# Kernel optimization log

Measured on AMD Instinct MI355X. Metric: run time of the kernel, lower is better.

The kernel has to match this reference:

```python
import jax, jax.numpy as jnp
import numpy as np

D_MODEL = 1024
N_HEADS = 16
D_K = D_MODEL // N_HEADS
FF_DIM = 4096
EPS = 1e-6
NEG = -1.0e9


def _layernorm(x, g, b):
    # torch: a_2 * (x - mean) / (std + eps) + b_2, std is unbiased (ddof=1)
    mean = jnp.mean(x, axis=-1, keepdims=True)
    std = jnp.std(x, axis=-1, keepdims=True, ddof=1)
    return g * (x - mean) / (std + EPS) + b


def setup_inputs() -> dict:
    key = jax.random.key(0)
    ks = jax.random.split(key, 8)
    s = 0.02
    x = jax.random.normal(ks[0], (2, 2048, D_MODEL), dtype=jnp.float32)
    mask = jnp.ones((2, 1, 1, 2048), dtype=jnp.int32)
    return {
        "x": x,
        "mask": mask,
        "wq": jax.random.normal(ks[1], (D_MODEL, D_MODEL), jnp.float32) * s,
        "wk": jax.random.normal(ks[2], (D_MODEL, D_MODEL), jnp.float32) * s,
        "wv": jax.random.normal(ks[3], (D_MODEL, D_MODEL), jnp.float32) * s,
        "wo": jax.random.normal(ks[4], (D_MODEL, D_MODEL), jnp.float32) * s,
        "bq": jnp.zeros((D_MODEL,), jnp.float32),
        "bk": jnp.zeros((D_MODEL,), jnp.float32),
        "bv": jnp.zeros((D_MODEL,), jnp.float32),
        "bo": jnp.zeros((D_MODEL,), jnp.float32),
        "w1": jax.random.normal(ks[5], (D_MODEL, FF_DIM), jnp.float32) * s,
        "b1": jnp.zeros((FF_DIM,), jnp.float32),
        "w2": jax.random.normal(ks[6], (FF_DIM, D_MODEL), jnp.float32) * s,
        "b2": jnp.zeros((D_MODEL,), jnp.float32),
        "ln1_g": jnp.ones((D_MODEL,), jnp.float32),
        "ln1_b": jnp.zeros((D_MODEL,), jnp.float32),
        "ln2_g": jnp.ones((D_MODEL,), jnp.float32),
        "ln2_b": jnp.zeros((D_MODEL,), jnp.float32),
    }


def reference(x, mask, wq, wk, wv, wo, bq, bk, bv, bo, w1, b1, w2, b2,
              ln1_g, ln1_b, ln2_g, ln2_b):
    B, S, _ = x.shape
    # --- sublayer 1: pre-norm self-attention with residual ---
    h = _layernorm(x, ln1_g, ln1_b)
    q = (h @ wq + bq).reshape(B, S, N_HEADS, D_K).transpose(0, 2, 1, 3)
    k = (h @ wk + bk).reshape(B, S, N_HEADS, D_K).transpose(0, 2, 1, 3)
    v = (h @ wv + bv).reshape(B, S, N_HEADS, D_K).transpose(0, 2, 1, 3)
    scores = jnp.einsum('bhqd,bhkd->bhqk', q, k) / np.sqrt(D_K).astype(np.float32)
    scores = jnp.where(mask == 0, NEG, scores)
    attn = jax.nn.softmax(scores, axis=-1)
    ctx = jnp.einsum('bhqk,bhkd->bhqd', attn, v)
    ctx = ctx.transpose(0, 2, 1, 3).reshape(B, S, D_MODEL)
    x = x + (ctx @ wo + bo)
    # --- sublayer 2: pre-norm FFN with residual ---
    h2 = _layernorm(x, ln2_g, ln2_b)
    ff = jax.nn.relu(h2 @ w1 + b1) @ w2 + b2
    return x + ff
```

## Files before the change

### kernel.cpp

```cpp
#include <hip/hip_runtime.h>

typedef unsigned short u16;
typedef unsigned int u32;
typedef __attribute__((ext_vector_type(8))) short bf16x8;
typedef __attribute__((ext_vector_type(4))) float f32x4;

__device__ __forceinline__ u16 f2bf(float f) {
  union { float f; unsigned int u; } x;
  x.f = f;
  unsigned int r = x.u + 0x7fffu + ((x.u >> 16) & 1u);
  return (u16)(r >> 16);
}

__device__ __forceinline__ float bf2f(u16 v) {
  union { unsigned int u; float f; } x;
  x.u = ((unsigned int)v) << 16;
  return x.f;
}

__device__ __forceinline__ u32 fbits(float f) {
  union { float f; u32 u; } x; x.f = f; return x.u;
}

__device__ __forceinline__ void async16(const u16* g, u16* l) {
  __builtin_amdgcn_global_load_lds((const __attribute__((address_space(1))) void*)g,
                                   (__attribute__((address_space(3))) void*)l, 16, 0, 0);
}

__device__ __forceinline__ void stage128x64(const u16* __restrict__ src, long row0, int k0,
                                            int ld, u16* lds, int wave, int lane) {
#pragma unroll
  for (int r = 0; r < 4; ++r) {
    int s = r * 256 + wave * 64 + lane;
    int row = s >> 3;
    int c = (s & 7) ^ (row & 7);
    async16(src + (row0 + row) * (long)ld + k0 + c * 8, lds + (r * 256 + wave * 64) * 8);
  }
}

__device__ __forceinline__ void stage_half512(const u16* __restrict__ src, long row0, int k0,
                                              int ld, u16* lbase, int wave, int lane) {
#pragma unroll
  for (int r = 0; r < 2; ++r) {
    int s = r * 512 + wave * 64 + lane;
    int row = s >> 3;
    int c = (s & 7) ^ (row & 7);
    async16(src + (row0 + row) * (long)ld + k0 + c * 8, lbase + (r * 512 + wave * 64) * 8);
  }
}

__device__ __forceinline__ void stage64x128(const u16* __restrict__ src, int col0, int ld,
                                            u16* lds, int wave, int lane) {
#pragma unroll
  for (int r = 0; r < 4; ++r) {
    int s = r * 256 + wave * 64 + lane;
    int row = s >> 4;
    int c = (s & 15) ^ (row & 15);
    async16(src + (long)row * ld + col0 + c * 8, lds + (r * 256 + wave * 64) * 8);
  }
}

__device__ __forceinline__ void ln_core(float4 v, const float* g, const float* b, int t,
                                        u16* outrow) {
  float s = v.x + v.y + v.z + v.w;
  float ss = v.x * v.x + v.y * v.y + v.z * v.z + v.w * v.w;
#pragma unroll
  for (int off = 32; off; off >>= 1) {
    s += __shfl_xor(s, off);
    ss += __shfl_xor(ss, off);
  }
  __shared__ float red[8];
  int wave = t >> 6, lane = t & 63;
  if (lane == 0) { red[wave] = s; red[wave + 4] = ss; }
  __syncthreads();
  float tot = red[0] + red[1] + red[2] + red[3];
  float tots = red[4] + red[5] + red[6] + red[7];
  float mean = tot * (1.0f / 1024.0f);
  float var = (tots - 1024.0f * mean * mean) * (1.0f / 1023.0f);
  var = fmaxf(var, 0.0f);
  float inv = 1.0f / (sqrtf(var) + 1e-6f);
  float4 gv = ((const float4*)g)[t];
  float4 bv = ((const float4*)b)[t];
  union { unsigned long long u64; u16 h[4]; } o;
  o.h[0] = f2bf(gv.x * (v.x - mean) * inv + bv.x);
  o.h[1] = f2bf(gv.y * (v.y - mean) * inv + bv.y);
  o.h[2] = f2bf(gv.z * (v.z - mean) * inv + bv.z);
  o.h[3] = f2bf(gv.w * (v.w - mean) * inv + bv.w);
  *(unsigned long long*)(outrow + t * 4) = o.u64;
}

__global__ __launch_bounds__(256) void prep(const float* __restrict__ wq,
                                            const float* __restrict__ wk,
                                            const float* __restrict__ wv,
                                            const float* __restrict__ wo,
                                            const float* __restrict__ w1,
                                            const float* __restrict__ w2,
                                            const float* __restrict__ x,
                                            const float* __restrict__ ln1_g,
                                            const float* __restrict__ ln1_b,
                                            u16* __restrict__ wqkvT,
                                            u16* __restrict__ w1T,
                                            u16* __restrict__ w2T,
                                            u16* __restrict__ hout) {
  const int bid = blockIdx.x;
  const int part = bid >> 12;
  const int local = bid & 4095;
  const int t = threadIdx.x;
  if (part == 1) {
    float4 v = ((const float4*)(x + (long)local * 1024))[t];
    ln_core(v, ln1_g, ln1_b, t, hout + (long)local * 1024);
    return;
  }
  __shared__ float tile[32][33];
  const float* src; u16* dst; int C, R, bx, by;
  if (part == 0) {
    int sub = local >> 10;
    src = sub == 0 ? wq : (sub == 1 ? wk : (sub == 2 ? wv : wo));
    dst = wqkvT + (long)sub * 1024 * 1024;
    C = 1024; R = 1024; bx = local & 31; by = (local >> 5) & 31;
  } else if (part == 2) {
    src = w1; dst = w1T; C = 4096; R = 1024; bx = local & 127; by = local >> 7;
  } else {
    src = w2; dst = w2T; C = 1024; R = 4096; bx = local & 31; by = local >> 5;
  }
  int c0 = bx * 32, r0 = by * 32;
  int tx = t & 31, ty = t >> 5;
#pragma unroll
  for (int i = 0; i < 32; i += 8)
    tile[ty + i][tx] = src[(long)(r0 + ty + i) * C + c0 + tx];
  __syncthreads();
#pragma unroll
  for (int i = 0; i < 32; i += 8)
    dst[(long)(c0 + ty + i) * R + r0 + tx] = f2bf(tile[tx][ty + i]);
}

__global__ __launch_bounds__(256) void ln_fuse(const float* x, const float* bres,
                                               const u16* p0, const u16* p1,
                                               const u16* p2, const u16* p3,
                                               const float* g, const float* b,
                                               float* yout, u16* hout) {
  int row = blockIdx.x, t = threadIdx.x;
  long base = (long)row * 1024;
  float4 xv = ((const float4*)(x + base))[t];
  float4 bo = ((const float4*)bres)[t];
  ushort4 a = ((const ushort4*)(p0 + base))[t];
  ushort4 c = ((const ushort4*)(p1 + base))[t];
  ushort4 d = ((const ushort4*)(p2 + base))[t];
  ushort4 e = ((const ushort4*)(p3 + base))[t];
  float4 y;
  y.x = xv.x + bo.x + (bf2f(a.x) + bf2f(c.x)) + (bf2f(d.x) + bf2f(e.x));
  y.y = xv.y + bo.y + (bf2f(a.y) + bf2f(c.y)) + (bf2f(d.y) + bf2f(e.y));
  y.z = xv.z + bo.z + (bf2f(a.z) + bf2f(c.z)) + (bf2f(d.z) + bf2f(e.z));
  y.w = xv.w + bo.w + (bf2f(a.w) + bf2f(c.w)) + (bf2f(d.w) + bf2f(e.w));
  ((float4*)(yout + base))[t] = y;
  ln_core(y, g, b, t, hout + base);
}

__global__ __launch_bounds__(256) void final_add(float* __restrict__ out,
                                                 const float* __restrict__ b2,
                                                 const u16* __restrict__ p0,
                                                 const u16* __restrict__ p1,
                                                 const u16* __restrict__ p2) {
  int row = blockIdx.x, t = threadIdx.x;
  long base = (long)row * 1024;
  float4 o = ((float4*)(out + base))[t];
  float4 bb = ((const float4*)b2)[t];
  ushort4 a = ((const ushort4*)(p0 + base))[t];
  ushort4 c = ((const ushort4*)(p1 + base))[t];
  ushort4 d = ((const ushort4*)(p2 + base))[t];
  o.x += bb.x + (bf2f(a.x) + bf2f(c.x)) + bf2f(d.x);
  o.y += bb.y + (bf2f(a.y) + bf2f(c.y)) + bf2f(d.y);
  o.z += bb.z + (bf2f(a.z) + bf2f(c.z)) + bf2f(d.z);
  o.w += bb.w + (bf2f(a.w) + bf2f(c.w)) + bf2f(d.w);
  ((float4*)(out + base))[t] = o;
}

template <int MODE, int SWZ>
__global__ __launch_bounds__(512, 1) void gemm8(const u16* __restrict__ A,
                                                const u16* __restrict__ Bt, int M, int N, int K,
                                                void* __restrict__ outp,
                                                const float* __restrict__ bias,
                                                const float* __restrict__ bias1,
                                                const float* __restrict__ bias2,
                                                u16* __restrict__ q_out, u16* __restrict__ k_out,
                                                u16* __restrict__ v_out) {
  __shared__ __align__(16) u16 lds[65536];
  (void)M;
  const int tid = threadIdx.x;
  const int wave = tid >> 6, lane = tid & 63;
  const int lane16 = lane & 15, quad = lane >> 4;
  const int wr2 = wave >> 2, wc2 = wave & 3;
  int bx = blockIdx.x, by = blockIdx.y;
  if (SWZ) {
    const int fid = by * gridDim.x + bx;
    const int xcd = fid & 7, slot = fid >> 3;
    const int nxh = gridDim.x >> 1;
    bx = (xcd & 1) * nxh + slot % nxh;
    by = (xcd >> 1) * 4 + slot / nxh;
  }
  const long m0 = (long)by * 256;
  const long n0 = (long)bx * 256;
  const int kLen = K / gridDim.z;
  const int kBeg = blockIdx.z * kLen;
  const int nT = kLen >> 6;

  u16* const ldsA = lds;
  u16* const ldsB = lds + 32768;

  const f32x4 fzero = {0.f, 0.f, 0.f, 0.f};
  f32x4 acc[2][2][4][2];
#pragma unroll
  for (int qa = 0; qa < 2; ++qa)
#pragma unroll
    for (int qb = 0; qb < 2; ++qb)
#pragma unroll
      for (int m = 0; m < 4; ++m)
#pragma unroll
        for (int n = 0; n < 2; ++n) acc[qa][qb][m][n] = fzero;

  stage_half512(A,  m0,       kBeg,      K, ldsA,                 wave, lane);
  stage_half512(Bt, n0,       kBeg,      K, ldsB,                 wave, lane);
  stage_half512(Bt, n0 + 128, kBeg,      K, ldsB + 8192,          wave, lane);
  stage_half512(A,  m0 + 128, kBeg,      K, ldsA + 8192,          wave, lane);
  stage_half512(A,  m0,       kBeg + 64, K, ldsA + 16384,         wave, lane);
  stage_half512(Bt, n0,       kBeg + 64, K, ldsB + 16384,         wave, lane);
  stage_half512(Bt, n0 + 128, kBeg + 64, K, ldsB + 16384 + 8192,  wave, lane);
  asm volatile("s_waitcnt vmcnt(10)" ::: "memory");
  asm volatile("s_barrier" ::: "memory");

  for (int t = 0; t < nT; ++t) {
    u16* const aB = ldsA + (t & 1) * 16384;
    u16* const bB = ldsB + (t & 1) * 16384;
    u16* const aN1 = ldsA + ((t + 1) & 1) * 16384;
    const int k1 = kBeg + (t + 1 < nT ? t + 1 : nT - 1) * 64;
    const int k2 = kBeg + (t + 2 < nT ? t + 2 : nT - 1) * 64;

    bf16x8 af[4][2], b0f[2][2], b1f[2][2];

#pragma unroll
    for (int m = 0; m < 4; ++m) {
      const int row = wr2 * 64 + m * 16 + lane16;
#pragma unroll
      for (int kk = 0; kk < 2; ++kk)
        af[m][kk] = *(const bf16x8*)(aB + row * 64 + (((kk * 4 + quad) ^ (row & 7)) << 3));
    }
#pragma unroll
    for (int n = 0; n < 2; ++n) {
      const int row = wc2 * 32 + n * 16 + lane16;
#pragma unroll
      for (int kk = 0; kk < 2; ++kk)
        b0f[n][kk] = *(const bf16x8*)(bB + row * 64 + (((kk * 4 + quad) ^ (row & 7)) << 3));
    }
    stage_half512(A, m0 + 128, k1, K, aN1 + 8192, wave, lane);
    asm volatile("s_barrier" ::: "memory");
    asm volatile("s_waitcnt lgkmcnt(0)" ::: "memory");
    __builtin_amdgcn_sched_barrier(0);
    __builtin_amdgcn_s_setprio(1);
#pragma unroll
    for (int m = 0; m < 4; ++m)
#pragma unroll
      for (int n = 0; n < 2; ++n) {
        acc[0][0][m][n] = __builtin_amdgcn_mfma_f32_16x16x32_bf16(af[m][0], b0f[n][0], acc[0][0][m][n], 0, 0, 0);
        acc[0][0][m][n] = __builtin_amdgcn_mfma_f32_16x16x32_bf16(af[m][1], b0f[n][1], acc[0][0][m][n], 0, 0, 0);
      }
    __builtin_amdgcn_s_setprio(0);
    asm volatile("s_waitcnt vmcnt(10)" ::: "memory");
    asm volatile("s_barrier" ::: "memory");

#pragma unroll
    for (int n = 0; n < 2; ++n) {
      const int row = 128 + wc2 * 32 + n * 16 + lane16;
#pragma unroll
      for (int kk = 0; kk < 2; ++kk)
        b1f[n][kk] = *(const bf16x8*)(bB + row * 64 + (((kk * 4 + quad) ^ (row & 7)) << 3));
    }
    stage_half512(A, m0, k2, K, aB, wave, lane);
    asm volatile("s_barrier" ::: "memory");
    asm volatile("s_waitcnt lgkmcnt(0)" ::: "memory");
    __builtin_amdgcn_sched_barrier(0);
    __builtin_amdgcn_s_setprio(1);
#pragma unroll
    for (int m = 0; m < 4; ++m)
#pragma unroll
      for (int n = 0; n < 2; ++n) {
        acc[0][1][m][n] = __builtin_amdgcn_mfma_f32_16x16x32_bf16(af[m][0], b1f[n][0], acc[0][1][m][n], 0, 0, 0);
        acc[0][1][m][n] = __builtin_amdgcn_mfma_f32_16x16x32_bf16(af[m][1], b1f[n][1], acc[0][1][m][n], 0, 0, 0);
      }
    __builtin_amdgcn_s_setprio(0);
    asm volatile("s_waitcnt vmcnt(10)" ::: "memory");
    asm volatile("s_barrier" ::: "memory");

#pragma unroll
    for (int m = 0; m < 4; ++m) {
      const int row = 128 + wr2 * 64 + m * 16 + lane16;
#pragma unroll
      for (int kk = 0; kk < 2; ++kk)
        af[m][kk] = *(const bf16x8*)(aB + row * 64 + (((kk * 4 + quad) ^ (row & 7)) << 3));
    }
    stage_half512(Bt, n0, k2, K, bB, wave, lane);
    asm volatile("s_barrier" ::: "memory");
    asm volatile("s_waitcnt lgkmcnt(0)" ::: "memory");
    __builtin_amdgcn_sched_barrier(0);
    __builtin_amdgcn_s_setprio(1);
#pragma unroll
    for (int m = 0; m < 4; ++m)
#pragma unroll
      for (int n = 0; n < 2; ++n) {
        acc[1][1][m][n] = __builtin_amdgcn_mfma_f32_16x16x32_bf16(af[m][0], b1f[n][0], acc[1][1][m][n], 0, 0, 0);
        acc[1][1][m][n] = __builtin_amdgcn_mfma_f32_16x16x32_bf16(af[m][1], b1f[n][1], acc[1][1][m][n], 0, 0, 0);
      }
    __builtin_amdgcn_s_setprio(0);
    asm volatile("s_waitcnt vmcnt(10)" ::: "memory");
    asm volatile("s_barrier" ::: "memory");

    stage_half512(Bt, n0 + 128, k2, K, bB + 8192, wave, lane);
    asm volatile("s_barrier" ::: "memory");
    __builtin_amdgcn_s_setprio(1);
#pragma unroll
    for (int m = 0; m < 4; ++m)
#pragma unroll
      for (int n = 0; n < 2; ++n) {
        acc[1][0][m][n] = __builtin_amdgcn_mfma_f32_16x16x32_bf16(af[m][0], b0f[n][0], acc[1][0][m][n], 0, 0, 0);
        acc[1][0][m][n] = __builtin_amdgcn_mfma_f32_16x16x32_bf16(af[m][1], b0f[n][1], acc[1][0][m][n], 0, 0, 0);
      }
    __builtin_amdgcn_s_setprio(0);
    asm volatile("s_waitcnt vmcnt(10)" ::: "memory");
    asm volatile("s_barrier" ::: "memory");
  }

  asm volatile("s_waitcnt vmcnt(0)" ::: "memory");

  if (MODE == 0) {
    const int sel = (int)(n0 >> 10);
    if (sel == 2) {
#pragma unroll
      for (int qa = 0; qa < 2; ++qa)
#pragma unroll
        for (int qb = 0; qb < 2; ++qb) {
          __syncthreads();
#pragma unroll
          for (int n = 0; n < 2; ++n) {
            const int lcol = wc2 * 32 + n * 16 + lane16;
            const float bvj = bias2[(int)(n0 - 2048) + qb * 128 + lcol];
#pragma unroll
            for (int m = 0; m < 4; ++m)
#pragma unroll
              for (int r = 0; r < 4; ++r) {
                const int lrow = wr2 * 64 + m * 16 + quad * 4 + r;
                lds[lcol * 136 + lrow] = f2bf(acc[qa][qb][m][n][r] + bvj);
              }
          }
          __syncthreads();
          const int lcol = tid >> 2, seg = tid & 3;
          const int cc = (int)(n0 - 2048) + qb * 128 + lcol;
          const int head = cc >> 6, d = cc & 63;
          const int bI = (int)((m0 + qa * 128) >> 11);
          const int s0 = (int)((m0 + qa * 128) & 2047);
          u16* dst = v_out + ((long)(bI * 16 + head) * 64 + d) * 2048 + s0 + seg * 32;
          const u16* s = lds + lcol * 136 + seg * 32;
#pragma unroll
          for (int c2 = 0; c2 < 4; ++c2) ((uint4*)dst)[c2] = ((const uint4*)s)[c2];
        }
      return;
    }
    u16* qk = sel == 0 ? q_out : k_out;
    const float* bb = sel == 0 ? bias : bias1;
#pragma unroll
    for (int qa = 0; qa < 2; ++qa)
#pragma unroll
      for (int qb = 0; qb < 2; ++qb)
#pragma unroll
        for (int n = 0; n < 2; ++n) {
          const int col = (int)n0 + qb * 128 + wc2 * 32 + n * 16 + lane16;
          const int cc = col & 1023;
          const float bv = bb[cc];
          const int head = cc >> 6, d = cc & 63;
#pragma unroll
          for (int m = 0; m < 4; ++m) {
            const int rw = (int)m0 + qa * 128 + wr2 * 64 + m * 16 + quad * 4;
#pragma unroll
            for (int r = 0; r < 4; ++r) {
              const int row = rw + r;
              const int bI = row >> 11, sS = row & 2047;
              const long bh = (long)bI * 16 + head;
              float vv = acc[qa][qb][m][n][r] + bv;
              if (sel == 0) vv *= 0.18033688f;
              qk[(bh * 2048 + sS) * 64 + d] = f2bf(vv);
            }
          }
        }
  } else if (MODE == 2) {
    u16* op = (u16*)outp;
#pragma unroll
    for (int qa = 0; qa < 2; ++qa)
#pragma unroll
      for (int qb = 0; qb < 2; ++qb)
#pragma unroll
        for (int n = 0; n < 2; ++n) {
          const int col = (int)n0 + qb * 128 + wc2 * 32 + n * 16 + lane16;
          const float bv = bias[col];
#pragma unroll
          for (int m = 0; m < 4; ++m) {
            const long rbase = ((long)m0 + qa * 128 + wr2 * 64 + m * 16 + quad * 4) * N + col;
#pragma unroll
            for (int r = 0; r < 4; ++r)
              op[rbase + (long)r * N] = f2bf(fmaxf(acc[qa][qb][m][n][r] + bv, 0.0f));
          }
        }
  } else {
    const int z = blockIdx.z;
    if (MODE == 3 && z == 3) {
      float* op = (float*)v_out;
#pragma unroll
      for (int qa = 0; qa < 2; ++qa)
#pragma unroll
        for (int qb = 0; qb < 2; ++qb)
#pragma unroll
          for (int n = 0; n < 2; ++n) {
            const int col = (int)n0 + qb * 128 + wc2 * 32 + n * 16 + lane16;
#pragma unroll
            for (int m = 0; m < 4; ++m) {
              const long rbase = ((long)m0 + qa * 128 + wr2 * 64 + m * 16 + quad * 4) * N + col;
#pragma unroll
              for (int r = 0; r < 4; ++r)
                unsafeAtomicAdd(op + rbase + (long)r * N, acc[qa][qb][m][n][r]);
            }
          }
    } else {
      u16* pp = z == 0 ? (u16*)outp : (z == 1 ? q_out : (z == 2 ? k_out : v_out));
#pragma unroll
      for (int qa = 0; qa < 2; ++qa)
#pragma unroll
        for (int qb = 0; qb < 2; ++qb)
#pragma unroll
          for (int n = 0; n < 2; ++n) {
            const int col = (int)n0 + qb * 128 + wc2 * 32 + n * 16 + lane16;
#pragma unroll
            for (int m = 0; m < 4; ++m) {
              const long rbase = ((long)m0 + qa * 128 + wr2 * 64 + m * 16 + quad * 4) * N + col;
#pragma unroll
              for (int r = 0; r < 4; ++r)
                pp[rbase + (long)r * N] = f2bf(acc[qa][qb][m][n][r]);
            }
          }
    }
  }
}

#define FA_C0 28.854239f
__global__ __launch_bounds__(256) void flash_attn(const u16* __restrict__ q,
                                                  const u16* __restrict__ k,
                                                  const u16* __restrict__ v,
                                                  const int* __restrict__ mask,
                                                  u16* __restrict__ ctx) {
  const int fid = blockIdx.y * 16 + blockIdx.x;
  const int xcd = fid & 7, slot = fid >> 3;
  const int bh = xcd * 4 + (slot >> 4);
  const int q0 = (slot & 15) * 128;
  const int b = bh >> 4, h = bh & 15;
  const int tid = threadIdx.x;
  const int wave = tid >> 6, lane = tid & 63;
  const int lane16 = lane & 15, quad = lane >> 4;

  const u16* qp = q + (long)bh * 2048 * 64;
  const u16* kp = k + (long)bh * 2048 * 64;
  const u16* vp = v + (long)bh * 64 * 2048;
  const int* mp = mask + b * 2048;

  __shared__ __align__(16) u16 ldsK[128 * 64];
  __shared__ __align__(16) u16 ldsVT[64 * 128];
  __shared__ __align__(16) u16 ldsP23[2 * 4096];
  __shared__ __align__(16) float ldsMask[128];
  __shared__ int ldsFlag[2];
  u16* myP = (wave < 2) ? (ldsK + wave * 4096) : (ldsP23 + (wave - 2) * 4096);

  bf16x8 qf[2][2];
#pragma unroll
  for (int g = 0; g < 2; ++g) {
    const long qrow = q0 + wave * 32 + g * 16 + lane16;
    qf[g][0] = *(const bf16x8*)(qp + qrow * 64 + quad * 8);
    qf[g][1] = *(const bf16x8*)(qp + qrow * 64 + 32 + quad * 8);
  }

  const f32x4 fzero = {0.f, 0.f, 0.f, 0.f};
  const f32x4 cC0 = {-FA_C0, -FA_C0, -FA_C0, -FA_C0};
  float l_loc[2] = {0.f, 0.f};
  f32x4 o_acc[2][4];
#pragma unroll
  for (int g = 0; g < 2; ++g)
#pragma unroll
    for (int j = 0; j < 4; ++j) o_acc[g][j] = fzero;

  const int xorm = (lane16 & 7) << 2;
  u16* const pw0 = myP + lane16 * 128;
  u16* const pw1 = myP + (16 + lane16) * 128;

  for (int kt = 0; kt < 2048; kt += 128) {
    stage128x64(kp, kt, 0, 64, ldsK, wave, lane);
    stage64x128(vp, kt, 2048, ldsVT, wave, lane);
    if (tid < 128) {
      int mv = mp[kt + tid];
      ldsMask[tid] = (mv == 0) ? -1.0e9f : 0.0f;
      unsigned long long bal = __ballot(mv != 0);
      if ((tid & 63) == 0) ldsFlag[tid >> 6] = (bal == ~0ull) ? 1 : 0;
    }
    __syncthreads();
    const bool allv = (ldsFlag[0] & ldsFlag[1]) != 0;

    f32x4 s_acc[8][2];
    __builtin_amdgcn_s_setprio(1);
#pragma unroll
    for (int j = 0; j < 8; ++j) {
      int row = j * 16 + lane16;
      int c0i = quad ^ (row & 7);
      int c1i = (4 + quad) ^ (row & 7);
      bf16x8 kf0 = *(const bf16x8*)(ldsK + row * 64 + c0i * 8);
      bf16x8 kf1 = *(const bf16x8*)(ldsK + row * 64 + c1i * 8);
#pragma unroll
      for (int g = 0; g < 2; ++g) {
        f32x4 sa = __builtin_amdgcn_mfma_f32_16x16x32_bf16(kf0, qf[g][0], cC0, 0, 0, 0);
        sa = __builtin_amdgcn_mfma_f32_16x16x32_bf16(kf1, qf[g][1], sa, 0, 0, 0);
        s_acc[j][g] = sa;
      }
    }
    __builtin_amdgcn_s_setprio(0);
    __syncthreads();

#pragma unroll
    for (int j = 0; j < 8; ++j) {
      int cw = ((4 * j + quad) ^ xorm) * 4;
#pragma unroll
      for (int g = 0; g < 2; ++g) {
        f32x4 sa = s_acc[j][g];
        if (!allv) {
          f32x4 mk = *(const f32x4*)(ldsMask + j * 16 + quad * 4);
          sa = sa + mk;
        }
        float p0 = __builtin_exp2f(sa[0]);
        float p1 = __builtin_exp2f(sa[1]);
        float p2 = __builtin_exp2f(sa[2]);
        float p3 = __builtin_exp2f(sa[3]);
        l_loc[g] += (p0 + p1) + (p2 + p3);
        uint2 pk;
        pk.x = __builtin_amdgcn_perm(fbits(p1), fbits(p0), 0x07060302u);
        pk.y = __builtin_amdgcn_perm(fbits(p3), fbits(p2), 0x07060302u);
        *(uint2*)((g ? pw1 : pw0) + cw) = pk;
      }
    }
    __builtin_amdgcn_s_setprio(1);
#pragma unroll
    for (int kk = 0; kk < 4; ++kk) {
      int cr = ((8 * kk + 2 * quad) ^ xorm) * 4;
      bf16x8 pf0 = *(const bf16x8*)(pw0 + cr);
      bf16x8 pf1 = *(const bf16x8*)(pw1 + cr);
#pragma unroll
      for (int jj = 0; jj < 4; ++jj) {
        int row = jj * 16 + lane16;
        int cv = (kk * 4 + quad) ^ (row & 15);
        bf16x8 vf = *(const bf16x8*)(ldsVT + row * 128 + cv * 8);
        o_acc[0][jj] = __builtin_amdgcn_mfma_f32_16x16x32_bf16(pf0, vf, o_acc[0][jj], 0, 0, 0);
        o_acc[1][jj] = __builtin_amdgcn_mfma_f32_16x16x32_bf16(pf1, vf, o_acc[1][jj], 0, 0, 0);
      }
    }
    __builtin_amdgcn_s_setprio(0);
    __syncthreads();
  }

  float lr[2][4];
#pragma unroll
  for (int g = 0; g < 2; ++g) {
    float l = l_loc[g];
#pragma unroll
    for (int off = 16; off < 64; off <<= 1) l += __shfl_xor(l, off);
    float linv = 1.0f / l;
#pragma unroll
    for (int r = 0; r < 4; ++r) lr[g][r] = __shfl(linv, quad * 4 + r);
  }

#pragma unroll
  for (int g = 0; g < 2; ++g)
#pragma unroll
    for (int jj = 0; jj < 4; ++jj)
#pragma unroll
      for (int r = 0; r < 4; ++r) {
        int sg = q0 + wave * 32 + g * 16 + quad * 4 + r;
        int d = jj * 16 + lane16;
        float val = o_acc[g][jj][r] * lr[g][r];
        ctx[((long)b * 2048 + sg) * 1024 + h * 64 + d] = f2bf(val);
      }
}

extern "C" void kernel_launch(void* const* d_in, const int* in_sizes, int n_in, void* d_out,
                              int out_size, void* d_ws, size_t ws_size, hipStream_t stream) {
  (void)in_sizes; (void)n_in; (void)out_size; (void)ws_size;
  const float* x  = (const float*)d_in[0];
  const int* mask = (const int*)d_in[1];
  const float* wq = (const float*)d_in[2];
  const float* wk = (const float*)d_in[3];
  const float* wv = (const float*)d_in[4];
  const float* wo = (const float*)d_in[5];
  const float* bq = (const float*)d_in[6];
  const float* bk = (const float*)d_in[7];
  const float* bv = (const float*)d_in[8];
  const float* bo = (const float*)d_in[9];
  const float* w1 = (const float*)d_in[10];
  const float* b1 = (const float*)d_in[11];
  const float* w2 = (const float*)d_in[12];
  const float* b2 = (const float*)d_in[13];
  const float* ln1_g = (const float*)d_in[14];
  const float* ln1_b = (const float*)d_in[15];
  const float* ln2_g = (const float*)d_in[16];
  const float* ln2_b = (const float*)d_in[17];
  float* out = (float*)d_out;

  u16* ws = (u16*)d_ws;
  u16* wqkvT = ws;
  u16* woT = wqkvT + 3072 * 1024;
  u16* w1T = woT + 1024 * 1024;
  u16* w2T = w1T + 4096 * 1024;
  u16* h   = w2T + 4096 * 1024;
  u16* qb  = h + 4096 * 1024;
  u16* kb  = qb + 4096 * 1024;
  u16* vb  = kb + 4096 * 1024;
  u16* ctx = vb + 4096 * 1024;
  u16* ffh = qb;

  prep<<<16384, 256, 0, stream>>>(wq, wk, wv, wo, w1, w2, x, ln1_g, ln1_b,
                                  wqkvT, w1T, w2T, h);

  gemm8<0, 1><<<dim3(12, 16), 512, 0, stream>>>(h, wqkvT, 4096, 3072, 1024, nullptr,
                                                bq, bk, bv, qb, kb, vb);

  flash_attn<<<dim3(16, 32), 256, 0, stream>>>(qb, kb, vb, mask, ctx);

  gemm8<1, 0><<<dim3(4, 16, 4), 512, 0, stream>>>(ctx, woT, 4096, 1024, 1024, h,
                                                  nullptr, nullptr, nullptr, qb, kb, vb);

  ln_fuse<<<4096, 256, 0, stream>>>(x, bo, h, qb, kb, vb, ln2_g, ln2_b, out, h);

  gemm8<2, 1><<<dim3(16, 16), 512, 0, stream>>>(h, w1T, 4096, 4096, 1024, ffh, b1,
                                                nullptr, nullptr, nullptr, nullptr, nullptr);

  gemm8<3, 0><<<dim3(4, 16, 4), 512, 0, stream>>>(ffh, w2T, 4096, 1024, 4096, ws,
                                                  nullptr, nullptr, nullptr, w1T, h, (u16*)out);

  final_add<<<4096, 256, 0, stream>>>(out, b2, ws, w1T, h);
}
```

Measured before the change: 360.0 us.

## Prefetch next K/V tile into registers and precompute per-tile mask flags

The attention loop now issues global loads for the next K and V tiles into registers before computing on the current tile, then writes them to LDS after a barrier. The goal is to hide global-load latency behind the MFMA and softmax work. Mask validity flags for all 16 key tiles are computed once up front, and the per-tile LDS mask staging and its barrier are removed. Mask values are read straight from global memory only when a tile is not fully valid. The trade-off is higher register pressure from holding eight uint4 values per thread, which may reduce occupancy. The manual waitcnt and barrier placement also has to be correct, since the P buffers alias ldsK.

Result: slower. 392.7 us (+9.1%).

```diff
diff --git a/kernel.cpp b/kernel.cpp
--- a/kernel.cpp
+++ b/kernel.cpp
@@ -470,9 +470,19 @@
   __shared__ __align__(16) u16 ldsK[128 * 64];
   __shared__ __align__(16) u16 ldsVT[64 * 128];
   __shared__ __align__(16) u16 ldsP23[2 * 4096];
-  __shared__ __align__(16) float ldsMask[128];
-  __shared__ int ldsFlag[2];
+  __shared__ int ldsFlag[16];
   u16* myP = (wave < 2) ? (ldsK + wave * 4096) : (ldsP23 + (wave - 2) * 4096);
+
+  {
+    int4 ma = ((const int4*)mp)[tid * 2];
+    int4 mb = ((const int4*)mp)[tid * 2 + 1];
+    bool ok = ma.x && ma.y && ma.z && ma.w && mb.x && mb.y && mb.z && mb.w;
+    unsigned long long bal = __ballot(ok);
+    if ((lane & 15) == 0) {
+      int i = lane >> 4;
+      ldsFlag[wave * 4 + i] = (((bal >> (16 * i)) & 0xFFFFull) == 0xFFFFull) ? 1 : 0;
+    }
+  }
 
   bf16x8 qf[2][2];
 #pragma unroll
@@ -495,17 +505,27 @@
   u16* const pw0 = myP + lane16 * 128;
   u16* const pw1 = myP + (16 + lane16) * 128;
 
+  stage128x64(kp, 0, 0, 64, ldsK, wave, lane);
+  stage64x128(vp, 0, 2048, ldsVT, wave, lane);
+  __syncthreads();
+
   for (int kt = 0; kt < 2048; kt += 128) {
-    stage128x64(kp, kt, 0, 64, ldsK, wave, lane);
-    stage64x128(vp, kt, 2048, ldsVT, wave, lane);
-    if (tid < 128) {
-      int mv = mp[kt + tid];
-      ldsMask[tid] = (mv == 0) ? -1.0e9f : 0.0f;
-      unsigned long long bal = __ballot(mv != 0);
-      if ((tid & 63) == 0) ldsFlag[tid >> 6] = (bal == ~0ull) ? 1 : 0;
-    }
-    __syncthreads();
-    const bool allv = (ldsFlag[0] & ldsFlag[1]) != 0;
+    const int ktn = (kt + 128 < 2048) ? kt + 128 : kt;
+
+    uint4 krg[4], vrg[4];
+#pragma unroll
+    for (int r = 0; r < 4; ++r) {
+      int s = r * 256 + wave * 64 + lane;
+      int row = s >> 3, c = (s & 7) ^ (row & 7);
+      krg[r] = *(const uint4*)(kp + (long)(ktn + row) * 64 + c * 8);
+    }
+#pragma unroll
+    for (int r = 0; r < 4; ++r) {
+      int s = r * 256 + wave * 64 + lane;
+      int row = s >> 4, c = (s & 15) ^ (row & 15);
+      vrg[r] = *(const uint4*)(vp + (long)row * 2048 + ktn + c * 8);
+    }
+    const bool allv = ldsFlag[kt >> 7] != 0;
 
     f32x4 s_acc[8][2];
     __builtin_amdgcn_s_setprio(1);
@@ -529,13 +549,18 @@
 #pragma unroll
     for (int j = 0; j < 8; ++j) {
       int cw = ((4 * j + quad) ^ xorm) * 4;
+      f32x4 mk = fzero;
+      if (!allv) {
+        int4 mi = *(const int4*)(mp + kt + j * 16 + quad * 4);
+        mk[0] = (mi.x == 0) ? -1.0e9f : 0.0f;
+        mk[1] = (mi.y == 0) ? -1.0e9f : 0.0f;
+        mk[2] = (mi.z == 0) ? -1.0e9f : 0.0f;
+        mk[3] = (mi.w == 0) ? -1.0e9f : 0.0f;
+      }
 #pragma unroll
       for (int g = 0; g < 2; ++g) {
         f32x4 sa = s_acc[j][g];
-        if (!allv) {
-          f32x4 mk = *(const f32x4*)(ldsMask + j * 16 + quad * 4);
-          sa = sa + mk;
-        }
+        if (!allv) sa = sa + mk;
         float p0 = __builtin_exp2f(sa[0]);
         float p1 = __builtin_exp2f(sa[1]);
         float p2 = __builtin_exp2f(sa[2]);
@@ -563,6 +588,19 @@
       }
     }
     __builtin_amdgcn_s_setprio(0);
+
+    asm volatile("s_waitcnt vmcnt(0)" ::: "memory");
+    asm volatile("s_barrier" ::: "memory");
+#pragma unroll
+    for (int r = 0; r < 4; ++r) {
+      int s = r * 256 + wave * 64 + lane;
+      *(uint4*)(ldsK + s * 8) = krg[r];
+    }
+#pragma unroll
+    for (int r = 0; r < 4; ++r) {
+      int s = r * 256 + wave * 64 + lane;
+      *(uint4*)(ldsVT + s * 8) = vrg[r];
+    }
     __syncthreads();
   }
 
```
